# Performance work log

Measured on AMD Instinct MI355X. Metric: run time of the kernel, lower is better.

The kernel has to match this reference:

```python
import jax, jax.numpy as jnp
import numpy as np

B, S, D = 4, 2048, 768
H = 12
HD = D // H
SCALE = HD ** -0.5


def setup_inputs() -> dict:
    key = jax.random.key(0)
    ks = jax.random.split(key, 5)
    std = D ** -0.5
    return {
        "hidden_states": jax.random.normal(ks[0], (B, S, D), dtype=jnp.float32),
        "qkv_w": jax.random.normal(ks[1], (3 * D, D), dtype=jnp.float32) * std,
        "qkv_b": jnp.zeros((3 * D,), dtype=jnp.float32),
        "proj_w": jax.random.normal(ks[2], (D, D), dtype=jnp.float32) * std,
        "proj_b": jnp.zeros((D,), dtype=jnp.float32),
    }


def reference(hidden_states, qkv_w, qkv_b, proj_w, proj_b):
    b, s, d = hidden_states.shape
    # fused QKV projection: [b,s,3d] -> [3,b,H,s,hd]
    mixed = hidden_states @ qkv_w.T + qkv_b
    mixed = mixed.reshape(b, s, 3, H, HD).transpose(2, 0, 3, 1, 4)
    q, k, v = mixed[0], mixed[1], mixed[2]
    # naive attention: full [b,H,s,s] score matrix, as in original module
    scores = jnp.einsum("bhqd,bhkd->bhqk", q, k) * SCALE
    probs = jax.nn.softmax(scores, axis=-1)
    ctx = jnp.einsum("bhqk,bhkd->bhqd", probs, v)
    ctx = ctx.transpose(0, 2, 1, 3).reshape(b, s, d)
    out = ctx @ proj_w.T + proj_b
    return out
```

## Files before the change

kernel.cpp:

```cpp
#include <hip/hip_runtime.h>
#include <hip/hip_bf16.h>

using short8   = __attribute__((ext_vector_type(8))) short;
using floatx4  = __attribute__((ext_vector_type(4))) float;
using floatx16 = __attribute__((ext_vector_type(16))) float;

#define KDIM 768
#define QSCALE 0.18033688011112042f
#define N1 (8192 * 768)
#define N2 (2304 * 768)
#define N3 (768 * 768)

__device__ __forceinline__ short f2bf(float f) {
    union { float f; unsigned u; } v; v.f = f;
    unsigned r = v.u + 0x7fffu + ((v.u >> 16) & 1u);
    return (short)(r >> 16);
}

__device__ __forceinline__ unsigned pack2bf(float a, float b) {
    __hip_bfloat162 h = __float22bfloat162_rn(float2{a, b});
    union { __hip_bfloat162 h; unsigned u; } c; c.h = h;
    return c.u;
}

__device__ __forceinline__ float fast_exp2(float x) {
#if __has_builtin(__builtin_amdgcn_exp2f)
    return __builtin_amdgcn_exp2f(x);
#else
    return exp2f(x);
#endif
}

__device__ __forceinline__ void async16(const void* g, void* l) {
    __builtin_amdgcn_global_load_lds((const __attribute__((address_space(1))) void*)g,
                                     (__attribute__((address_space(3))) void*)l, 16, 0, 0);
}

__global__ void cvt_all(const float* __restrict__ a, const float* __restrict__ b,
                        const float* __restrict__ c, short* __restrict__ oa,
                        short* __restrict__ ob, short* __restrict__ oc) {
    int i = (blockIdx.x * blockDim.x + threadIdx.x) * 4;
    const float* src; short* dst;
    if (i < N1)            { src = a + i;            dst = oa + i; }
    else if (i < N1 + N2)  { src = b + (i - N1);     dst = ob + (i - N1); }
    else if (i < N1+N2+N3) { src = c + (i - N1 - N2); dst = oc + (i - N1 - N2); }
    else return;
    float4 v = *(const float4*)src;
    short4 o;
    o.x = f2bf(v.x); o.y = f2bf(v.y); o.z = f2bf(v.z); o.w = f2bf(v.w);
    *(short4*)dst = o;
}

__global__ __launch_bounds__(256) void gemm_qkv(
    const short* __restrict__ X, const short* __restrict__ W,
    const float* __restrict__ bias,
    short* __restrict__ Qb, short* __restrict__ Kb, short* __restrict__ Vb)
{
    __shared__ short As[128 * 32];
    __shared__ short Bs[128 * 32];
    int tid = threadIdx.x;
    int w = tid >> 6, l = tid & 63;
    int lane16 = l & 15, quad = l >> 4;
    int wm = w & 1, wn = w >> 1;
    int m0 = blockIdx.y * 128, n0 = blockIdx.x * 128;

    floatx4 acc[4][4] = {};

    int srow = w * 32 + (l >> 2);
    int scol = (l & 3) * 8;
    const short* Xg = X + (size_t)(m0 + srow) * KDIM + scol;
    const short* Wg = W + (size_t)(n0 + srow) * KDIM + scol;
    short* AsW = As + (w * 32) * 32;
    short* BsW = Bs + (w * 32) * 32;

    for (int kb = 0; kb < KDIM; kb += 32) {
        __syncthreads();
        async16(Xg + kb,              AsW);
        async16(Xg + kb + 16 * KDIM,  AsW + 16 * 32);
        async16(Wg + kb,              BsW);
        async16(Wg + kb + 16 * KDIM,  BsW + 16 * 32);
        __syncthreads();
        short8 a[4], b[4];
#pragma unroll
        for (int mt = 0; mt < 4; mt++) a[mt] = *(const short8*)(As + (wm * 64 + mt * 16 + lane16) * 32 + quad * 8);
#pragma unroll
        for (int nt = 0; nt < 4; nt++) b[nt] = *(const short8*)(Bs + (wn * 64 + nt * 16 + lane16) * 32 + quad * 8);
#pragma unroll
        for (int mt = 0; mt < 4; mt++)
#pragma unroll
            for (int nt = 0; nt < 4; nt++)
                acc[mt][nt] = __builtin_amdgcn_mfma_f32_16x16x32_bf16(a[mt], b[nt], acc[mt][nt], 0, 0, 0);
    }

#pragma unroll
    for (int mt = 0; mt < 4; mt++) {
        int row = m0 + wm * 64 + mt * 16 + quad * 4;
#pragma unroll
        for (int nt = 0; nt < 4; nt++) {
            int col = n0 + wn * 64 + nt * 16 + lane16;
            int qkv = (col >= 1536) ? 2 : ((col >= 768) ? 1 : 0);
            int rem = col - qkv * 768;
            int h = rem >> 6, e = rem & 63;
            short* dst = (qkv == 0) ? Qb : ((qkv == 1) ? Kb : Vb);
            float sc = (qkv == 0) ? (float)QSCALE : 1.0f;
            float bv = bias[col];
#pragma unroll
            for (int r = 0; r < 4; r++) {
                int i  = row + r;
                int b_ = i >> 11, s_ = i & 2047;
                dst[(((size_t)(b_ * 12 + h)) * 2048 + s_) * 64 + e] = f2bf((acc[mt][nt][r] + bv) * sc);
            }
        }
    }
}

__global__ __launch_bounds__(256) void transpose_v(
    const short* __restrict__ Vb, short* __restrict__ Vt)
{
    __shared__ short T[64 * 66];
    int tid = threadIdx.x;
    int s0 = blockIdx.x * 64, bh = blockIdx.y;
    const short* src = Vb + (size_t)bh * 2048 * 64;
    short* dst = Vt + (size_t)bh * 64 * 2048;

#pragma unroll
    for (int i = 0; i < 2; i++) {
        int slot = i * 256 + tid;
        int s_loc = slot >> 3, ec = slot & 7;
        short8 v = *(const short8*)(src + (size_t)(s0 + s_loc) * 64 + ec * 8);
        *(short8*)(T + s_loc * 66 + ec * 8) = v;
    }
    __syncthreads();
#pragma unroll
    for (int i = 0; i < 2; i++) {
        int slot = i * 256 + tid;
        int e_loc = slot >> 3, sc = slot & 7;
        short8 o;
#pragma unroll
        for (int j = 0; j < 8; j++) {
            int p = sc * 8 + j;
            int kp = (p & 0x33) | ((p & 4) << 1) | ((p & 8) >> 1);
            o[j] = T[kp * 66 + e_loc];
        }
        *(short8*)(dst + (size_t)e_loc * 2048 + s0 + sc * 8) = o;
    }
}

__global__ __launch_bounds__(256, 3) void attn(
    const short* __restrict__ Qb, const short* __restrict__ Kb,
    const short* __restrict__ Vt, short* __restrict__ Ctx)
{
    __shared__ short Ks[512 * 8];
    __shared__ short Vs[512 * 8];
    int tid = threadIdx.x, w = tid >> 6, l = tid & 63;
    int l32 = l & 31, half = l >> 5;
    int qt = blockIdx.x, bh = blockIdx.y;
    const short* Qh  = Qb + (size_t)bh * 2048 * 64;
    const short* Kh  = Kb + (size_t)bh * 2048 * 64;
    const short* Vth = Vt + (size_t)bh * 64 * 2048;
    int qbase = qt * 128 + w * 32;

    const short* kSrc[2];
    const short* vSrc[2];
    short* kDst[2];
    short* vDst[2];
#pragma unroll
    for (int i = 0; i < 2; i++) {
        int slot = i * 256 + tid;
        int row = slot >> 3;
        int g = (slot & 7) ^ (row & 7);
        kSrc[i] = Kh + (size_t)row * 64 + g * 8;
        vSrc[i] = Vth + (size_t)row * 2048 + g * 8;
        kDst[i] = Ks + (size_t)(i * 256 + w * 64) * 8;
        vDst[i] = Vs + (size_t)(i * 256 + w * 64) * 8;
    }

    short8 qf[4];
#pragma unroll
    for (int ks = 0; ks < 4; ks++)
        qf[ks] = *(const short8*)(Qh + (size_t)(qbase + l32) * 64 + ks * 16 + half * 8);

    float lsum = 0.f;
    floatx16 acc[2] = {};
    int sw = l32 & 7;

    for (int kt = 0; kt < 32; kt++) {
        __syncthreads();
#pragma unroll
        for (int i = 0; i < 2; i++) {
            async16(kSrc[i] + (size_t)kt * 64 * 64, kDst[i]);
            async16(vSrc[i] + (size_t)kt * 64,      vDst[i]);
        }
        __syncthreads();

        floatx16 s[2];
#pragma unroll
        for (int nt = 0; nt < 2; nt++) {
            floatx16 c = {};
            int rowb = (nt * 32 + l32) * 8;
#pragma unroll
            for (int ks = 0; ks < 4; ks++) {
                short8 kf = *(const short8*)(Ks + (size_t)(rowb + ((ks * 2 + half) ^ sw)) * 8);
                c = __builtin_amdgcn_mfma_f32_32x32x16_bf16(kf, qf[ks], c, 0, 0, 0);
            }
            s[nt] = c;
        }

        union { short8 s8; unsigned u[4]; } pa[4];
#pragma unroll
        for (int nt = 0; nt < 2; nt++)
#pragma unroll
            for (int r = 0; r < 16; r += 2) {
                float p0 = fast_exp2(s[nt][r]);
                float p1 = fast_exp2(s[nt][r + 1]);
                lsum += p0 + p1;
                pa[2 * nt + (r >> 3)].u[(r & 7) >> 1] = pack2bf(p0, p1);
            }

#pragma unroll
        for (int nt = 0; nt < 2; nt++) {
            int rowb = (nt * 32 + l32) * 8;
#pragma unroll
            for (int ks = 0; ks < 4; ks++) {
                short8 vf = *(const short8*)(Vs + (size_t)(rowb + ((ks * 2 + half) ^ sw)) * 8);
                acc[nt] = __builtin_amdgcn_mfma_f32_32x32x16_bf16(pa[ks].s8, vf, acc[nt], 0, 0, 0);
            }
        }
    }

    float denom = lsum + __shfl_xor(lsum, 32);
    float inv_self = 1.0f / denom;

    int b_ = bh / 12, h = bh % 12;
#pragma unroll
    for (int nt = 0; nt < 2; nt++)
#pragma unroll
        for (int r = 0; r < 16; r++) {
            int qloc = (r & 3) + 8 * (r >> 2) + 4 * half;
            float invq = __shfl(inv_self, qloc);
            int q = qbase + qloc;
            int e = nt * 32 + l32;
            Ctx[((size_t)(b_ * 2048 + q)) * 768 + h * 64 + e] = f2bf(acc[nt][r] * invq);
        }
}

__global__ __launch_bounds__(256) void gemm_out(
    const short* __restrict__ Ctx, const short* __restrict__ W,
    const float* __restrict__ bias, float* __restrict__ out)
{
    __shared__ short As[128 * 32];
    __shared__ short Bs[128 * 32];
    int tid = threadIdx.x;
    int w = tid >> 6, l = tid & 63;
    int lane16 = l & 15, quad = l >> 4;
    int wm = w & 1, wn = w >> 1;
    int m0 = blockIdx.y * 128, n0 = blockIdx.x * 128;

    floatx4 acc[4][4] = {};

    int srow = w * 32 + (l >> 2);
    int scol = (l & 3) * 8;
    const short* Xg = Ctx + (size_t)(m0 + srow) * KDIM + scol;
    const short* Wg = W + (size_t)(n0 + srow) * KDIM + scol;
    short* AsW = As + (w * 32) * 32;
    short* BsW = Bs + (w * 32) * 32;

    for (int kb = 0; kb < KDIM; kb += 32) {
        __syncthreads();
        async16(Xg + kb,             AsW);
        async16(Xg + kb + 16 * KDIM, AsW + 16 * 32);
        async16(Wg + kb,             BsW);
        async16(Wg + kb + 16 * KDIM, BsW + 16 * 32);
        __syncthreads();
        short8 a[4], b[4];
#pragma unroll
        for (int mt = 0; mt < 4; mt++) a[mt] = *(const short8*)(As + (wm * 64 + mt * 16 + lane16) * 32 + quad * 8);
#pragma unroll
        for (int nt = 0; nt < 4; nt++) b[nt] = *(const short8*)(Bs + (wn * 64 + nt * 16 + lane16) * 32 + quad * 8);
#pragma unroll
        for (int mt = 0; mt < 4; mt++)
#pragma unroll
            for (int nt = 0; nt < 4; nt++)
                acc[mt][nt] = __builtin_amdgcn_mfma_f32_16x16x32_bf16(a[mt], b[nt], acc[mt][nt], 0, 0, 0);
    }

#pragma unroll
    for (int mt = 0; mt < 4; mt++) {
        int row = m0 + wm * 64 + mt * 16 + quad * 4;
#pragma unroll
        for (int nt = 0; nt < 4; nt++) {
            int col = n0 + wn * 64 + nt * 16 + lane16;
            float bv = bias[col];
#pragma unroll
            for (int r = 0; r < 4; r++)
                out[(size_t)(row + r) * 768 + col] = acc[mt][nt][r] + bv;
        }
    }
}

extern "C" void kernel_launch(void* const* d_in, const int* in_sizes, int n_in,
                              void* d_out, int out_size, void* d_ws, size_t ws_size,
                              hipStream_t stream) {
    const float* hs     = (const float*)d_in[0];
    const float* qkv_w  = (const float*)d_in[1];
    const float* qkv_b  = (const float*)d_in[2];
    const float* proj_w = (const float*)d_in[3];
    const float* proj_b = (const float*)d_in[4];
    float* out = (float*)d_out;

    short* Xb  = (short*)d_ws;
    short* W1b = Xb  + (size_t)8192 * 768;
    short* W2b = W1b + (size_t)2304 * 768;
    short* Qb  = W2b + (size_t)768 * 768;
    short* Kb  = Qb  + (size_t)8192 * 768;
    short* Vb  = Kb  + (size_t)8192 * 768;
    short* Ctx = Vb  + (size_t)8192 * 768;
    short* Vt  = Xb;

    int ntot = (N1 + N2 + N3) / 4;
    cvt_all<<<(ntot + 255) / 256, 256, 0, stream>>>(hs, qkv_w, proj_w, Xb, W1b, W2b);

    gemm_qkv<<<dim3(18, 64), 256, 0, stream>>>(Xb, W1b, qkv_b, Qb, Kb, Vb);
    transpose_v<<<dim3(32, 48), 256, 0, stream>>>(Vb, Vt);
    attn<<<dim3(16, 48), 256, 0, stream>>>(Qb, Kb, Vt, Ctx);
    gemm_out<<<dim3(6, 64), 256, 0, stream>>>(Ctx, W2b, proj_b, out);
}
```

Measured before the change: 224.2 us.

## Double-buffer attention K/V tiles and halve output-GEMM M tile

The attention kernel now keeps two LDS buffers for K and V. It prefetches the next key tile while computing on the current one, which cuts the loop from two barriers per iteration to one. The aim is to overlap global-to-LDS transfer with MFMA and exp work, at the cost of doubled LDS use that may reduce occupancy. Separately, the output projection GEMM uses a 64-row M tile instead of 128, doubling the grid to give more blocks per CU at the cost of less B-tile reuse.

```diff
diff --git a/kernel.cpp b/kernel.cpp
--- a/kernel.cpp
+++ b/kernel.cpp
@@ -150,8 +150,8 @@
     const short* __restrict__ Qb, const short* __restrict__ Kb,
     const short* __restrict__ Vt, short* __restrict__ Ctx)
 {
-    __shared__ short Ks[512 * 8];
-    __shared__ short Vs[512 * 8];
+    __shared__ short Ks[2][512 * 8];
+    __shared__ short Vs[2][512 * 8];
     int tid = threadIdx.x, w = tid >> 6, l = tid & 63;
     int l32 = l & 31, half = l >> 5;
     int qt = blockIdx.x, bh = blockIdx.y;
@@ -171,8 +171,14 @@
         int g = (slot & 7) ^ (row & 7);
         kSrc[i] = Kh + (size_t)row * 64 + g * 8;
         vSrc[i] = Vth + (size_t)row * 2048 + g * 8;
-        kDst[i] = Ks + (size_t)(i * 256 + w * 64) * 8;
-        vDst[i] = Vs + (size_t)(i * 256 + w * 64) * 8;
+        kDst[i] = &Ks[0][0] + (size_t)(i * 256 + w * 64) * 8;
+        vDst[i] = &Vs[0][0] + (size_t)(i * 256 + w * 64) * 8;
+    }
+
+#pragma unroll
+    for (int i = 0; i < 2; i++) {
+        async16(kSrc[i], kDst[i]);
+        async16(vSrc[i], vDst[i]);
     }
 
     short8 qf[4];
@@ -184,14 +190,23 @@
     floatx16 acc[2] = {};
     int sw = l32 & 7;
 
+    __syncthreads();
+
     for (int kt = 0; kt < 32; kt++) {
-        __syncthreads();
-#pragma unroll
-        for (int i = 0; i < 2; i++) {
-            async16(kSrc[i] + (size_t)kt * 64 * 64, kDst[i]);
-            async16(vSrc[i] + (size_t)kt * 64,      vDst[i]);
-        }
-        __syncthreads();
+        int cur = kt & 1, nxt = kt + 1;
+        const short* Kcur = &Ks[cur][0];
+        const short* Vcur = &Vs[cur][0];
+
+        if (nxt < 32) {
+            int nb = nxt & 1;
+            size_t kOff = (size_t)nxt * 4096;
+            size_t vOff = (size_t)nxt * 64;
+#pragma unroll
+            for (int i = 0; i < 2; i++) {
+                async16(kSrc[i] + kOff, kDst[i] + (size_t)nb * 4096);
+                async16(vSrc[i] + vOff, vDst[i] + (size_t)nb * 4096);
+            }
+        }
 
         floatx16 s[2];
 #pragma unroll
@@ -200,7 +215,7 @@
             int rowb = (nt * 32 + l32) * 8;
 #pragma unroll
             for (int ks = 0; ks < 4; ks++) {
-                short8 kf = *(const short8*)(Ks + (size_t)(rowb + ((ks * 2 + half) ^ sw)) * 8);
+                short8 kf = *(const short8*)(Kcur + (size_t)(rowb + ((ks * 2 + half) ^ sw)) * 8);
                 c = __builtin_amdgcn_mfma_f32_32x32x16_bf16(kf, qf[ks], c, 0, 0, 0);
             }
             s[nt] = c;
@@ -222,10 +237,12 @@
             int rowb = (nt * 32 + l32) * 8;
 #pragma unroll
             for (int ks = 0; ks < 4; ks++) {
-                short8 vf = *(const short8*)(Vs + (size_t)(rowb + ((ks * 2 + half) ^ sw)) * 8);
+                short8 vf = *(const short8*)(Vcur + (size_t)(rowb + ((ks * 2 + half) ^ sw)) * 8);
                 acc[nt] = __builtin_amdgcn_mfma_f32_32x32x16_bf16(pa[ks].s8, vf, acc[nt], 0, 0, 0);
             }
         }
+
+        __syncthreads();
     }
 
     float denom = lsum + __shfl_xor(lsum, 32);
@@ -248,45 +265,44 @@
     const short* __restrict__ Ctx, const short* __restrict__ W,
     const float* __restrict__ bias, float* __restrict__ out)
 {
-    __shared__ short As[128 * 32];
+    __shared__ short As[64 * 32];
     __shared__ short Bs[128 * 32];
     int tid = threadIdx.x;
     int w = tid >> 6, l = tid & 63;
     int lane16 = l & 15, quad = l >> 4;
     int wm = w & 1, wn = w >> 1;
-    int m0 = blockIdx.y * 128, n0 = blockIdx.x * 128;
-
-    floatx4 acc[4][4] = {};
-
-    int srow = w * 32 + (l >> 2);
-    int scol = (l & 3) * 8;
+    int m0 = blockIdx.y * 64, n0 = blockIdx.x * 128;
+
+    floatx4 acc[2][4] = {};
+
+    int srow = tid >> 2;
+    int scol = (tid & 3) * 8;
     const short* Xg = Ctx + (size_t)(m0 + srow) * KDIM + scol;
     const short* Wg = W + (size_t)(n0 + srow) * KDIM + scol;
-    short* AsW = As + (w * 32) * 32;
-    short* BsW = Bs + (w * 32) * 32;
+    short* AsW = As + (w * 16) * 32;
+    short* BsW = Bs + (w * 16) * 32;
 
     for (int kb = 0; kb < KDIM; kb += 32) {
         __syncthreads();
         async16(Xg + kb,             AsW);
-        async16(Xg + kb + 16 * KDIM, AsW + 16 * 32);
         async16(Wg + kb,             BsW);
-        async16(Wg + kb + 16 * KDIM, BsW + 16 * 32);
-        __syncthreads();
-        short8 a[4], b[4];
-#pragma unroll
-        for (int mt = 0; mt < 4; mt++) a[mt] = *(const short8*)(As + (wm * 64 + mt * 16 + lane16) * 32 + quad * 8);
+        async16(Wg + kb + 64 * KDIM, BsW + 64 * 32);
+        __syncthreads();
+        short8 a[2], b[4];
+#pragma unroll
+        for (int mt = 0; mt < 2; mt++) a[mt] = *(const short8*)(As + (wm * 32 + mt * 16 + lane16) * 32 + quad * 8);
 #pragma unroll
         for (int nt = 0; nt < 4; nt++) b[nt] = *(const short8*)(Bs + (wn * 64 + nt * 16 + lane16) * 32 + quad * 8);
 #pragma unroll
-        for (int mt = 0; mt < 4; mt++)
+        for (int mt = 0; mt < 2; mt++)
 #pragma unroll
             for (int nt = 0; nt < 4; nt++)
                 acc[mt][nt] = __builtin_amdgcn_mfma_f32_16x16x32_bf16(a[mt], b[nt], acc[mt][nt], 0, 0, 0);
     }
 
 #pragma unroll
-    for (int mt = 0; mt < 4; mt++) {
-        int row = m0 + wm * 64 + mt * 16 + quad * 4;
+    for (int mt = 0; mt < 2; mt++) {
+        int row = m0 + wm * 32 + mt * 16 + quad * 4;
 #pragma unroll
         for (int nt = 0; nt < 4; nt++) {
             int col = n0 + wn * 64 + nt * 16 + lane16;
@@ -323,5 +339,5 @@
     gemm_qkv<<<dim3(18, 64), 256, 0, stream>>>(Xb, W1b, qkv_b, Qb, Kb, Vb);
     transpose_v<<<dim3(32, 48), 256, 0, stream>>>(Vb, Vt);
     attn<<<dim3(16, 48), 256, 0, stream>>>(Qb, Kb, Vt, Ctx);
-    gemm_out<<<dim3(6, 64), 256, 0, stream>>>(Ctx, W2b, proj_b, out);
-}
+    gemm_out<<<dim3(6, 128), 256, 0, stream>>>(Ctx, W2b, proj_b, out);
+}
```

Result: slower. 230.5 us (+2.8%).
